# Optimization experiments

Measured on AMD Instinct MI355X. Metric: run time of the kernel, lower is better.

## Reference

```python
import jax, jax.numpy as jnp
import numpy as np

EMBED = 256
HEADS = 8
LEVELS = 3
POINTS = 4
MLP = 4
SS = np.array([[100, 100], [50, 50], [25, 25]], np.int32)  # (H, W) per level


def setup_inputs() -> dict:
    key = jax.random.key(0)
    ks = jax.random.split(key, 12)
    B, Q = 2, 128 * 128
    NV = int((SS[:, 0] * SS[:, 1]).sum())
    C = EMBED
    F = C * MLP
    s = 0.02

    def w(k, shape):
        return jax.random.normal(k, shape, jnp.float32) * s

    return dict(
        query=jax.random.normal(ks[0], (B, Q, C), jnp.float32),
        value=jax.random.normal(ks[1], (B, NV, C), jnp.float32),
        query_pos=jax.random.normal(ks[2], (B, Q, C), jnp.float32),
        ref_pts=jax.random.uniform(ks[3], (B, Q, 2), jnp.float32),
        spatial_shapes=SS,
        level_start_index=np.concatenate([[0], np.cumsum(SS[:, 0] * SS[:, 1])[:-1]]).astype(np.int32),
        ln1_g=jnp.ones(C), ln1_b=jnp.zeros(C),
        ln2_g=jnp.ones(C), ln2_b=jnp.zeros(C),
        W_value=w(ks[4], (C, C)), b_value=jnp.zeros(C),
        W_off=w(ks[5], (C, HEADS * LEVELS * POINTS * 2)), b_off=w(ks[6], (HEADS * LEVELS * POINTS * 2,)),
        W_attn=w(ks[7], (C, HEADS * LEVELS * POINTS)), b_attn=jnp.zeros(HEADS * LEVELS * POINTS),
        W_out=w(ks[8], (C, C)), b_out=jnp.zeros(C),
        W_ffn1=w(ks[9], (C, F)), b_ffn1=jnp.zeros(F),
        W_ffn2=w(ks[10], (F, C)), b_ffn2=jnp.zeros(C),
    )


def _layernorm(x, g, b, eps=1e-5):
    m = x.mean(-1, keepdims=True)
    v = ((x - m) ** 2).mean(-1, keepdims=True)
    return (x - m) * jax.lax.rsqrt(v + eps) * g + b


def _bilinear(v, loc, Hl, Wl):
    # v: [BH, Hl*Wl, d]; loc: [BH, Q, P, 2] normalized to [0,1].
    # grid_sample(align_corners=False, padding=zeros): pixel = loc*size - 0.5
    BH, Q, P, _ = loc.shape
    d = v.shape[-1]
    x = loc[..., 0] * Wl - 0.5
    y = loc[..., 1] * Hl - 0.5
    x0f = jnp.floor(x)
    y0f = jnp.floor(y)
    lx = x - x0f
    ly = y - y0f
    x0 = x0f.astype(jnp.int32)
    y0 = y0f.astype(jnp.int32)

    def gather(xi, yi):
        valid = ((xi >= 0) & (xi < Wl) & (yi >= 0) & (yi < Hl)).astype(v.dtype)
        idx = jnp.clip(yi, 0, Hl - 1) * Wl + jnp.clip(xi, 0, Wl - 1)
        g = jnp.take_along_axis(v, idx.reshape(BH, Q * P, 1), axis=1).reshape(BH, Q, P, d)
        return g * valid[..., None]

    w00 = (1 - lx) * (1 - ly)
    w01 = lx * (1 - ly)
    w10 = (1 - lx) * ly
    w11 = lx * ly
    return (gather(x0, y0) * w00[..., None] + gather(x0 + 1, y0) * w01[..., None]
            + gather(x0, y0 + 1) * w10[..., None] + gather(x0 + 1, y0 + 1) * w11[..., None])


def _forward(query, value, query_pos, ref_pts, spatial_shapes,
             ln1_g, ln1_b, ln2_g, ln2_b,
             W_value, b_value, W_off, b_off, W_attn, b_attn, W_out, b_out,
             W_ffn1, b_ffn1, W_ffn2, b_ffn2):
    B, Q, C = query.shape
    Hh, L, P = HEADS, LEVELS, POINTS
    d = C // Hh
    ss = np.asarray(spatial_shapes)
    starts = np.concatenate([[0], np.cumsum(ss[:, 0] * ss[:, 1])])

    # pre-norm + positional embedding (MSDeformAttn adds query_pos)
    qn = _layernorm(query, ln1_g, ln1_b)
    q = qn + query_pos

    # value projection, split heads
    v = (value @ W_value + b_value).reshape(B, -1, Hh, d)

    off = (q @ W_off + b_off).reshape(B, Q, Hh, L, P, 2)
    aw = jax.nn.softmax((q @ W_attn + b_attn).reshape(B, Q, Hh, L * P), axis=-1)
    aw = aw.reshape(B, Q, Hh, L, P)

    # offset normalizer is (W, H) per level
    normalizer = jnp.asarray(ss[:, ::-1].copy(), jnp.float32)
    # bev_value path: ref_pts broadcast over levels
    loc = ref_pts[:, :, None, None, None, :] + off / normalizer[None, None, None, :, None, :]

    out = jnp.zeros((B * Hh, Q, d), query.dtype)
    for l in range(L):
        Hl, Wl = int(ss[l, 0]), int(ss[l, 1])
        v_l = v[:, starts[l]:starts[l + 1]].transpose(0, 2, 1, 3).reshape(B * Hh, Hl * Wl, d)
        loc_l = loc[:, :, :, l].transpose(0, 2, 1, 3, 4).reshape(B * Hh, Q, P, 2)
        sampled = _bilinear(v_l, loc_l, Hl, Wl)  # [BH, Q, P, d]
        w_l = aw[:, :, :, l].transpose(0, 2, 1, 3).reshape(B * Hh, Q, P)
        out = out + (sampled * w_l[..., None]).sum(2)

    out = out.reshape(B, Hh, Q, d).transpose(0, 2, 1, 3).reshape(B, Q, C)
    x = query + (out @ W_out + b_out)

    h = _layernorm(x, ln2_g, ln2_b)
    x = x + (jax.nn.gelu(h @ W_ffn1 + b_ffn1, approximate=False) @ W_ffn2 + b_ffn2)
    return x


def reference(query, value, query_pos, ref_pts, spatial_shapes, level_start_index,
              ln1_g, ln1_b, ln2_g, ln2_b,
              W_value, b_value, W_off, b_off, W_attn, b_attn, W_out, b_out,
              W_ffn1, b_ffn1, W_ffn2, b_ffn2):
    return _forward(query, value, query_pos, ref_pts, spatial_shapes,
                    ln1_g, ln1_b, ln2_g, ln2_b,
                    W_value, b_value, W_off, b_off, W_attn, b_attn, W_out, b_out,
                    W_ffn1, b_ffn1, W_ffn2, b_ffn2)
```

## Files before the change

kernel.cpp:

```cpp
#include <hip/hip_runtime.h>
#include <hip/hip_bf16.h>

#define BQ      2
#define QLEN    16384
#define CDIM    256
#define HEADS   8
#define LEV     3
#define PTS     4
#define DHEAD   32
#define NVTOT   13125
#define FDIM    1024
#define NTOK    (BQ*QLEN)
#define MROWS_V (BQ*NVTOT)
#define NPROJ   288

typedef __attribute__((ext_vector_type(8))) short short8;
typedef __attribute__((ext_vector_type(4))) float floatx4;
typedef unsigned long long u64;

typedef const __attribute__((address_space(1))) unsigned int gu32;
typedef __attribute__((address_space(3))) unsigned int lu32;

__device__ __forceinline__ int imin(int a, int b){ return a<b?a:b; }
__device__ __forceinline__ int imax(int a, int b){ return a>b?a:b; }

__device__ __forceinline__ float bf2f(unsigned short u){ return __uint_as_float((unsigned)u << 16); }
__device__ __forceinline__ unsigned short f2bf(float f)
{
    __hip_bfloat16 h = __float2bfloat16(f);
    return *(unsigned short*)&h;
}
__device__ __forceinline__ u64 pack4(float4 v)
{
    return (u64)f2bf(v.x) | ((u64)f2bf(v.y) << 16)
         | ((u64)f2bf(v.z) << 32) | ((u64)f2bf(v.w) << 48);
}
__device__ __forceinline__ float4 unpack4(u64 c)
{
    float4 v;
    v.x = bf2f((unsigned short)(c));
    v.y = bf2f((unsigned short)(c >> 16));
    v.z = bf2f((unsigned short)(c >> 32));
    v.w = bf2f((unsigned short)(c >> 48));
    return v;
}

__device__ __forceinline__ float gelu_f(float x)
{
    float u2 = x * x;
    float a  = x * fmaf(0.0713548163f, u2, 1.5957691216f);
    float e  = __expf(a);
    float r  = __builtin_amdgcn_rcpf(e + 1.0f);
    return fmaf(-x, r, x);
}

__device__ __forceinline__ void ln_core(float4 v, const float* __restrict__ pos, int tok,
                                        const float* __restrict__ g, const float* __restrict__ b,
                                        int lane, __hip_bfloat16* __restrict__ out)
{
    float s = v.x + v.y + v.z + v.w;
    #pragma unroll
    for (int o = 32; o > 0; o >>= 1) s += __shfl_down(s, o);
    s = __shfl(s, 0);
    float mean = s * (1.0f / 256.0f);
    float4 c; c.x = v.x - mean; c.y = v.y - mean; c.z = v.z - mean; c.w = v.w - mean;
    float q2 = c.x*c.x + c.y*c.y + c.z*c.z + c.w*c.w;
    #pragma unroll
    for (int o = 32; o > 0; o >>= 1) q2 += __shfl_down(q2, o);
    q2 = __shfl(q2, 0);
    float rstd = rsqrtf(q2 * (1.0f / 256.0f) + 1e-5f);
    float4 gg = ((const float4*)g)[lane];
    float4 bb = ((const float4*)b)[lane];
    float4 o4;
    o4.x = c.x * rstd * gg.x + bb.x;
    o4.y = c.y * rstd * gg.y + bb.y;
    o4.z = c.z * rstd * gg.z + bb.z;
    o4.w = c.w * rstd * gg.w + bb.w;
    if (pos) {
        float4 p = ((const float4*)(pos + (size_t)tok * CDIM))[lane];
        o4.x += p.x; o4.y += p.y; o4.z += p.z; o4.w += p.w;
    }
    *(u64*)(out + (size_t)tok * CDIM + lane * 4) = pack4(o4);
}

#define WT_BLOCKS  2946
#define CVT_BLOCKS 6563
#define LN_BLOCKS  8192

__global__ __launch_bounds__(256)
void prep_k(const float* __restrict__ Wv,  const float* __restrict__ Woff,
            const float* __restrict__ Wat, const float* __restrict__ Wout,
            const float* __restrict__ W1,  const float* __restrict__ W2,
            const float* __restrict__ boff, const float* __restrict__ bat,
            const float* __restrict__ value, const float* __restrict__ query,
            const float* __restrict__ qpos,  const float* __restrict__ ln1g,
            const float* __restrict__ ln1b,
            __hip_bfloat16* __restrict__ o_v,  __hip_bfloat16* __restrict__ o_c,
            __hip_bfloat16* __restrict__ o_out,
            __hip_bfloat16* __restrict__ o_1,  __hip_bfloat16* __restrict__ o_2,
            float* __restrict__ o_bc,
            __hip_bfloat16* __restrict__ vbf,  __hip_bfloat16* __restrict__ qbf)
{
    int bx = blockIdx.x;
    if (bx < WT_BLOCKS) {
        int gid = bx * 256 + threadIdx.x;
        if (gid < 65536) {
            int idx = gid, n = idx >> 8, k = idx & 255;
            o_v[idx] = __float2bfloat16(Wv[(size_t)k * 256 + n]);
        } else if (gid < 163840) {
            int idx = gid - 65536, n = idx >> 8, k = idx & 255;
            float v = 0.0f;
            if (n < 192)       v = Woff[(size_t)k * 192 + n];
            else if (n < 288)  v = Wat[(size_t)k * 96 + (n - 192)];
            o_c[idx] = __float2bfloat16(v);
        } else if (gid < 229376) {
            int idx = gid - 163840, n = idx >> 8, k = idx & 255;
            o_out[idx] = __float2bfloat16(Wout[(size_t)k * 256 + n]);
        } else if (gid < 491520) {
            int idx = gid - 229376, n = idx >> 8, k = idx & 255;
            o_1[idx] = __float2bfloat16(W1[(size_t)k * 1024 + n]);
        } else if (gid < 753664) {
            int idx = gid - 491520, n = idx >> 10, k = idx & 1023;
            o_2[idx] = __float2bfloat16(W2[(size_t)k * 256 + n]);
        } else if (gid < 753952) {
            int idx = gid - 753664;
            o_bc[idx] = (idx < 192) ? boff[idx] : bat[idx - 192];
        }
    } else if (bx < WT_BLOCKS + CVT_BLOCKS) {
        int i = (bx - WT_BLOCKS) * 256 + threadIdx.x;
        if (i < MROWS_V * CDIM / 4) {
            float4 v = ((const float4*)value)[i];
            *(u64*)(vbf + (size_t)i * 4) = pack4(v);
        }
    } else {
        int tok  = (bx - WT_BLOCKS - CVT_BLOCKS) * 4 + (threadIdx.x >> 6);
        int lane = threadIdx.x & 63;
        float4 v = ((const float4*)(query + (size_t)tok * CDIM))[lane];
        ln_core(v, qpos, tok, ln1g, ln1b, lane, qbf);
    }
}

__global__ __launch_bounds__(256)
void ln2_k(const __hip_bfloat16* __restrict__ x, const float* __restrict__ g,
           const float* __restrict__ b, __hip_bfloat16* __restrict__ out)
{
    int tok  = blockIdx.x * 4 + (threadIdx.x >> 6);
    int lane = threadIdx.x & 63;
    float4 v = unpack4(((const u64*)(x + (size_t)tok * CDIM))[lane]);
    ln_core(v, nullptr, tok, g, b, lane, out);
}

enum { EP_PLAIN_BF16 = 0, EP_GELU_BF16 = 1, EP_RES_F2BF = 2, EP_RES_BF2F = 3 };

__global__ __launch_bounds__(256)
void mm_k(const __hip_bfloat16* __restrict__ A, const __hip_bfloat16* __restrict__ Bt,
          const float* __restrict__ bias, const void* __restrict__ res,
          void* __restrict__ Cout, int M, int N, int K, int mode)
{
    __shared__ float4 smem4[2048];
    __hip_bfloat16* Ws = (__hip_bfloat16*)smem4;
    __hip_bfloat16* Ts = (__hip_bfloat16*)smem4 + 128*64;
    u64* st = (u64*)smem4;
    int t = threadIdx.x;
    int lane = t & 63;
    int wave = t >> 6;
    int wm = wave >> 1, wn = wave & 1;
    int lm = lane & 15, lk = lane >> 4;
    int m0 = blockIdx.x * 128;
    int n0 = blockIdx.y * 128;

    floatx4 acc[4][4];
    #pragma unroll
    for (int i = 0; i < 4; i++)
        #pragma unroll
        for (int j = 0; j < 4; j++) acc[i][j] = (floatx4)0.0f;

    for (int kt = 0; kt < K; kt += 64) {
        #pragma unroll
        for (int i = 0; i < 4; i++) {
            int cc  = i * 256 + t;
            int row = cc >> 3;
            int c   = cc & 7;
            int kc  = c ^ (row & 7);
            int ra  = m0 + row; if (ra >= M) ra = M - 1;
            const __hip_bfloat16* gw = Bt + (size_t)(n0 + row) * K + kt + kc * 8;
            const __hip_bfloat16* gt = A  + (size_t)ra * K + kt + kc * 8;
            __builtin_amdgcn_global_load_lds((gu32*)gw, (lu32*)(Ws + cc * 8), 16, 0, 0);
            __builtin_amdgcn_global_load_lds((gu32*)gt, (lu32*)(Ts + cc * 8), 16, 0, 0);
        }
        __syncthreads();
        #pragma unroll
        for (int ks = 0; ks < 2; ks++) {
            short8 wf[4], tf[4];
            #pragma unroll
            for (int i = 0; i < 4; i++) {
                int rw = wn * 64 + i * 16 + lm;
                int cw = (ks * 4 + lk) ^ (rw & 7);
                wf[i] = *(const short8*)(Ws + (rw * 8 + cw) * 8);
                int rt = wm * 64 + i * 16 + lm;
                int ct = (ks * 4 + lk) ^ (rt & 7);
                tf[i] = *(const short8*)(Ts + (rt * 8 + ct) * 8);
            }
            #pragma unroll
            for (int i = 0; i < 4; i++)
                #pragma unroll
                for (int j = 0; j < 4; j++)
                    acc[i][j] = __builtin_amdgcn_mfma_f32_16x16x32_bf16(wf[i], tf[j], acc[i][j], 0, 0, 0);
        }
        __syncthreads();
    }

    #pragma unroll
    for (int i = 0; i < 4; i++) {
        int chan = n0 + wn * 64 + i * 16 + lk * 4;
        float4 b4 = make_float4(0.f, 0.f, 0.f, 0.f);
        if (chan < N) b4 = *(const float4*)(bias + chan);
        int c4 = wn * 16 + i * 4 + lk;
        #pragma unroll
        for (int j = 0; j < 4; j++) {
            int tl = wm * 64 + j * 16 + lm;
            float4 v;
            v.x = acc[i][j][0] + b4.x;
            v.y = acc[i][j][1] + b4.y;
            v.z = acc[i][j][2] + b4.z;
            v.w = acc[i][j][3] + b4.w;
            st[tl * 32 + (c4 ^ (tl & 31))] = pack4(v);
        }
    }
    __syncthreads();

    int rel = (t & 31) * 4;
    int c4r = t & 31;
    #pragma unroll
    for (int it = 0; it < 16; it++) {
        int tl   = it * 8 + (t >> 5);
        int tok  = m0 + tl;
        int chan = n0 + rel;
        if (tok >= M || chan >= N) continue;
        u64 chunk = st[tl * 32 + (c4r ^ (tl & 31))];
        if (mode == EP_PLAIN_BF16) {
            *(u64*)((__hip_bfloat16*)Cout + (size_t)tok * N + chan) = chunk;
        } else if (mode == EP_GELU_BF16) {
            float4 v = unpack4(chunk);
            v.x = gelu_f(v.x); v.y = gelu_f(v.y); v.z = gelu_f(v.z); v.w = gelu_f(v.w);
            *(u64*)((__hip_bfloat16*)Cout + (size_t)tok * N + chan) = pack4(v);
        } else if (mode == EP_RES_F2BF) {
            float4 v = unpack4(chunk);
            float4 rr = *(const float4*)((const float*)res + (size_t)tok * N + chan);
            v.x += rr.x; v.y += rr.y; v.z += rr.z; v.w += rr.w;
            *(u64*)((__hip_bfloat16*)Cout + (size_t)tok * N + chan) = pack4(v);
        } else {
            float4 v = unpack4(chunk);
            float4 rr = unpack4(*(const u64*)((const __hip_bfloat16*)res + (size_t)tok * N + chan));
            v.x += rr.x; v.y += rr.y; v.z += rr.z; v.w += rr.w;
            *(float4*)((float*)Cout + (size_t)tok * N + chan) = v;
        }
    }
}

__global__ __launch_bounds__(256, 6)
void sample_k(const __hip_bfloat16* __restrict__ v, const __hip_bfloat16* __restrict__ cbuf,
              const float* __restrict__ ref, __hip_bfloat16* __restrict__ out)
{
    __shared__ int4   metaIdx[4 * 104];
    __shared__ float4 metaW[4 * 104];

    int wid  = threadIdx.x >> 6;
    int lane = threadIdx.x & 63;
    int t    = blockIdx.x * 4 + wid;
    int b    = t >> 14;
    float rx = ref[(size_t)t * 2 + 0];
    float ry = ref[(size_t)t * 2 + 1];
    const __hip_bfloat16* crow = cbuf + (size_t)t * NPROJ;

    #pragma unroll
    for (int rnd = 0; rnd < 2; rnd++) {
        int slot = rnd * 64 + lane;
        int h = slot >> 4, p = slot & 15;
        int pc = imin(p, 11);
        unsigned upk = *(const unsigned*)(crow + h * 24 + pc * 2);
        float ox = bf2f((unsigned short)upk);
        float oy = bf2f((unsigned short)(upk >> 16));
        float logit = bf2f(*(const unsigned short*)(crow + 192 + h * 12 + pc));
        float mx = logit;
        #pragma unroll
        for (int o = 8; o > 0; o >>= 1) mx = fmaxf(mx, __shfl_xor(mx, o, 16));
        float e = (p < 12) ? __expf(logit - mx) : 0.0f;
        float ssum = e;
        #pragma unroll
        for (int o = 8; o > 0; o >>= 1) ssum += __shfl_xor(ssum, o, 16);
        float aw = e * __builtin_amdgcn_rcpf(ssum);

        if (p < 12) {
            int l = p >> 2;
            float fS = (l == 0) ? 100.0f : ((l == 1) ? 50.0f : 25.0f);
            int   Wl = (l == 0) ? 100 : ((l == 1) ? 50 : 25);
            int   st = (l == 0) ? 0 : ((l == 1) ? 10000 : 12500);
            float x = fmaf(rx, fS, ox) - 0.5f;
            float y = fmaf(ry, fS, oy) - 0.5f;
            float x0f = floorf(x), y0f = floorf(y);
            float fx = x - x0f, fy = y - y0f;
            int x0 = (int)x0f, y0 = (int)y0f;
            int x1 = x0 + 1,  y1 = y0 + 1;
            int cx0 = imin(imax(x0, 0), Wl - 1), cx1 = imin(imax(x1, 0), Wl - 1);
            int cy0 = imin(imax(y0, 0), Wl - 1), cy1 = imin(imax(y1, 0), Wl - 1);
            float vx0 = (x0 >= 0 && x0 < Wl) ? 1.0f : 0.0f;
            float vx1 = (x1 >= 0 && x1 < Wl) ? 1.0f : 0.0f;
            float vy0 = (y0 >= 0 && y0 < Wl) ? 1.0f : 0.0f;
            float vy1 = (y1 >= 0 && y1 < Wl) ? 1.0f : 0.0f;
            int s = wid * 104 + h * 13 + p;
            metaIdx[s] = make_int4((st + cy0 * Wl + cx0) << 9, (st + cy0 * Wl + cx1) << 9,
                                   (st + cy1 * Wl + cx0) << 9, (st + cy1 * Wl + cx1) << 9);
            metaW[s] = make_float4((1.0f - fx) * (1.0f - fy) * aw * vx0 * vy0,
                                   fx * (1.0f - fy) * aw * vx1 * vy0,
                                   (1.0f - fx) * fy * aw * vx0 * vy1,
                                   fx * fy * aw * vx1 * vy1);
        }
    }
    __syncthreads();

    int h  = lane >> 3;
    int bs = __builtin_amdgcn_readfirstlane(b);
    const char* vb = (const char*)(v + (size_t)bs * NVTOT * CDIM);
    int hoff = lane * 8;
    int sB   = wid * 104 + h * 13;
    float4 acc = {0.0f, 0.0f, 0.0f, 0.0f};

    int4   miA = metaIdx[sB + 0];
    float4 mwA = metaW[sB + 0];
    u64 a0 = *(const u64*)(vb + (unsigned)(miA.x + hoff));
    u64 a1 = *(const u64*)(vb + (unsigned)(miA.y + hoff));
    u64 a2 = *(const u64*)(vb + (unsigned)(miA.z + hoff));
    u64 a3 = *(const u64*)(vb + (unsigned)(miA.w + hoff));
    int4   miB = metaIdx[sB + 1];
    float4 mwB = metaW[sB + 1];
    u64 b0 = *(const u64*)(vb + (unsigned)(miB.x + hoff));
    u64 b1 = *(const u64*)(vb + (unsigned)(miB.y + hoff));
    u64 b2 = *(const u64*)(vb + (unsigned)(miB.z + hoff));
    u64 b3 = *(const u64*)(vb + (unsigned)(miB.w + hoff));

    #pragma unroll
    for (int p = 0; p < 12; p++) {
        int pn = (p < 10) ? (p + 2) : 11;
        int4   miN = metaIdx[sB + pn];
        float4 mwN = metaW[sB + pn];
        u64 n0 = *(const u64*)(vb + (unsigned)(miN.x + hoff));
        u64 n1 = *(const u64*)(vb + (unsigned)(miN.y + hoff));
        u64 n2 = *(const u64*)(vb + (unsigned)(miN.z + hoff));
        u64 n3 = *(const u64*)(vb + (unsigned)(miN.w + hoff));

        {
            unsigned d0 = (unsigned)a0, d1 = (unsigned)(a0 >> 32);
            acc.x = fmaf(mwA.x, __uint_as_float(d0 << 16), acc.x);
            acc.y = fmaf(mwA.x, __uint_as_float(d0 & 0xffff0000u), acc.y);
            acc.z = fmaf(mwA.x, __uint_as_float(d1 << 16), acc.z);
            acc.w = fmaf(mwA.x, __uint_as_float(d1 & 0xffff0000u), acc.w);
        }
        {
            unsigned d0 = (unsigned)a1, d1 = (unsigned)(a1 >> 32);
            acc.x = fmaf(mwA.y, __uint_as_float(d0 << 16), acc.x);
            acc.y = fmaf(mwA.y, __uint_as_float(d0 & 0xffff0000u), acc.y);
            acc.z = fmaf(mwA.y, __uint_as_float(d1 << 16), acc.z);
            acc.w = fmaf(mwA.y, __uint_as_float(d1 & 0xffff0000u), acc.w);
        }
        {
            unsigned d0 = (unsigned)a2, d1 = (unsigned)(a2 >> 32);
            acc.x = fmaf(mwA.z, __uint_as_float(d0 << 16), acc.x);
            acc.y = fmaf(mwA.z, __uint_as_float(d0 & 0xffff0000u), acc.y);
            acc.z = fmaf(mwA.z, __uint_as_float(d1 << 16), acc.z);
            acc.w = fmaf(mwA.z, __uint_as_float(d1 & 0xffff0000u), acc.w);
        }
        {
            unsigned d0 = (unsigned)a3, d1 = (unsigned)(a3 >> 32);
            acc.x = fmaf(mwA.w, __uint_as_float(d0 << 16), acc.x);
            acc.y = fmaf(mwA.w, __uint_as_float(d0 & 0xffff0000u), acc.y);
            acc.z = fmaf(mwA.w, __uint_as_float(d1 << 16), acc.z);
            acc.w = fmaf(mwA.w, __uint_as_float(d1 & 0xffff0000u), acc.w);
        }

        a0 = b0; a1 = b1; a2 = b2; a3 = b3; mwA = mwB;
        b0 = n0; b1 = n1; b2 = n2; b3 = n3; mwB = mwN;
    }
    *(u64*)(out + (size_t)t * CDIM + lane * 4) = pack4(acc);
}

extern "C" void kernel_launch(void* const* d_in, const int* in_sizes, int n_in,
                              void* d_out, int out_size, void* d_ws, size_t ws_size,
                              hipStream_t stream)
{
    const float* query = (const float*)d_in[0];
    const float* value = (const float*)d_in[1];
    const float* qpos  = (const float*)d_in[2];
    const float* ref   = (const float*)d_in[3];
    const float* ln1g  = (const float*)d_in[6];
    const float* ln1b  = (const float*)d_in[7];
    const float* ln2g  = (const float*)d_in[8];
    const float* ln2b  = (const float*)d_in[9];
    const float* Wv    = (const float*)d_in[10];
    const float* bv    = (const float*)d_in[11];
    const float* Woff  = (const float*)d_in[12];
    const float* boff  = (const float*)d_in[13];
    const float* Wat   = (const float*)d_in[14];
    const float* bat   = (const float*)d_in[15];
    const float* Wout  = (const float*)d_in[16];
    const float* bout  = (const float*)d_in[17];
    const float* W1    = (const float*)d_in[18];
    const float* b1    = (const float*)d_in[19];
    const float* W2    = (const float*)d_in[20];
    const float* b2    = (const float*)d_in[21];
    float* out = (float*)d_out;
    char*  ws  = (char*)d_ws;

    const size_t MB = 1024 * 1024;
    __hip_bfloat16* Wvt   = (__hip_bfloat16*)(ws + 0);
    __hip_bfloat16* Wct   = (__hip_bfloat16*)(ws + 131072);
    __hip_bfloat16* Woutt = (__hip_bfloat16*)(ws + 327680);
    __hip_bfloat16* W1t   = (__hip_bfloat16*)(ws + 458752);
    __hip_bfloat16* W2t   = (__hip_bfloat16*)(ws + 983040);
    float*          bcomb = (float*)(ws + 1507328);
    __hip_bfloat16* qbf   = (__hip_bfloat16*)(ws + 2  * MB);
    __hip_bfloat16* aoutb = (__hip_bfloat16*)(ws + 19 * MB);
    __hip_bfloat16* vbf   = (__hip_bfloat16*)(ws + 36 * MB);
    __hip_bfloat16* vbuf  = (__hip_bfloat16*)(ws + 50 * MB);
    __hip_bfloat16* xbf   = (__hip_bfloat16*)(ws + 64 * MB);
    __hip_bfloat16* cbuf  = (__hip_bfloat16*)(ws + 81 * MB);
    __hip_bfloat16* gbf   = (__hip_bfloat16*)(ws + 100 * MB);
    __hip_bfloat16* hbf   = qbf;

    prep_k<<<WT_BLOCKS + CVT_BLOCKS + LN_BLOCKS, 256, 0, stream>>>(
        Wv, Woff, Wat, Wout, W1, W2, boff, bat, value, query, qpos, ln1g, ln1b,
        Wvt, Wct, Woutt, W1t, W2t, bcomb, vbf, qbf);
    mm_k<<<dim3((MROWS_V + 127) / 128, 2), 256, 0, stream>>>(
        vbf, Wvt, bv, nullptr, vbuf, MROWS_V, 256, 256, EP_PLAIN_BF16);
    mm_k<<<dim3(NTOK / 128, 3), 256, 0, stream>>>(
        qbf, Wct, bcomb, nullptr, cbuf, NTOK, NPROJ, 256, EP_PLAIN_BF16);
    sample_k<<<NTOK / 4, 256, 0, stream>>>(vbuf, cbuf, ref, aoutb);
    mm_k<<<dim3(NTOK / 128, 2), 256, 0, stream>>>(
        aoutb, Woutt, bout, query, xbf, NTOK, 256, 256, EP_RES_F2BF);
    ln2_k<<<NTOK / 4, 256, 0, stream>>>(xbf, ln2g, ln2b, hbf);
    mm_k<<<dim3(NTOK / 128, 8), 256, 0, stream>>>(
        hbf, W1t, b1, nullptr, gbf, NTOK, FDIM, 256, EP_GELU_BF16);
    mm_k<<<dim3(NTOK / 128, 2), 256, 0, stream>>>(
        gbf, W2t, b2, xbf, out, NTOK, 256, 1024, EP_RES_BF2F);
}
```

Measured before the change: 355.1 us.

## Fuse FFN up-projection, GELU and down-projection into one kernel

Replaces the two FFN GEMM launches with a single kernel. Each 128-token block keeps its LN2 output tile in LDS, computes 128-wide chunks of the hidden layer with GELU into a double-buffered LDS tile, and accumulates the down-projection in registers, adding bias and residual at the end. This removes the round trip of the 1024-wide bf16 hidden activation through global memory. In exchange it needs 128KB of dynamic LDS per block, which limits occupancy, and only 256 blocks are launched. Weight fragments are loaded straight from global memory in every chunk without LDS staging.

```diff
diff --git a/kernel.cpp b/kernel.cpp
--- a/kernel.cpp
+++ b/kernel.cpp
@@ -258,6 +258,152 @@
     }
 }
 
+__global__ __launch_bounds__(512, 2)
+void ffn_k(const __hip_bfloat16* __restrict__ h,
+           const __hip_bfloat16* __restrict__ W1t,
+           const float* __restrict__ b1,
+           const __hip_bfloat16* __restrict__ W2t,
+           const float* __restrict__ b2,
+           const __hip_bfloat16* __restrict__ xres,
+           float* __restrict__ out)
+{
+    extern __shared__ char smem_dyn[];
+    __hip_bfloat16* As = (__hip_bfloat16*)smem_dyn;
+
+    int t    = threadIdx.x;
+    int lane = t & 63;
+    int wave = t >> 6;
+    int wm   = wave >> 2;
+    int wn   = wave & 3;
+    int lm   = lane & 15, lk = lane >> 4;
+    int m0   = blockIdx.x * 128;
+
+    #pragma unroll
+    for (int i = 0; i < 8; i++) {
+        int cc  = i * 512 + t;
+        int kt  = cc >> 10;
+        int rem = cc & 1023;
+        int row = rem >> 3;
+        int c   = rem & 7;
+        int kc  = c ^ (row & 7);
+        const __hip_bfloat16* src = h + (size_t)(m0 + row) * 256 + kt * 64 + kc * 8;
+        __builtin_amdgcn_global_load_lds((gu32*)src, (lu32*)(As + cc * 8), 16, 0, 0);
+    }
+
+    floatx4 acc2[4][4];
+    #pragma unroll
+    for (int i = 0; i < 4; i++)
+        #pragma unroll
+        for (int j = 0; j < 4; j++) acc2[i][j] = (floatx4)0.0f;
+
+    __syncthreads();
+
+    #pragma unroll 1
+    for (int fc = 0; fc < 8; fc++) {
+        int f0 = fc * 128;
+        __hip_bfloat16* gs = (__hip_bfloat16*)(smem_dyn + 65536 + (fc & 1) * 32768);
+
+        floatx4 acc1[2][4];
+        #pragma unroll
+        for (int i = 0; i < 2; i++)
+            #pragma unroll
+            for (int j = 0; j < 4; j++) acc1[i][j] = (floatx4)0.0f;
+
+        short8 w1f[8][2];
+        #pragma unroll
+        for (int kt = 0; kt < 4; kt++)
+            #pragma unroll
+            for (int ks = 0; ks < 2; ks++)
+                #pragma unroll
+                for (int i = 0; i < 2; i++)
+                    w1f[kt * 2 + ks][i] = *(const short8*)(W1t
+                        + (size_t)(f0 + wn * 32 + i * 16 + lm) * 256
+                        + kt * 64 + ks * 32 + lk * 8);
+
+        #pragma unroll
+        for (int kt = 0; kt < 4; kt++) {
+            #pragma unroll
+            for (int ks = 0; ks < 2; ks++) {
+                short8 tf[4];
+                #pragma unroll
+                for (int j = 0; j < 4; j++) {
+                    int rt = wm * 64 + j * 16 + lm;
+                    int ct = (ks * 4 + lk) ^ (rt & 7);
+                    tf[j] = *(const short8*)(As + (kt * 1024 + rt * 8 + ct) * 8);
+                }
+                #pragma unroll
+                for (int i = 0; i < 2; i++)
+                    #pragma unroll
+                    for (int j = 0; j < 4; j++)
+                        acc1[i][j] = __builtin_amdgcn_mfma_f32_16x16x32_bf16(
+                            w1f[kt * 2 + ks][i], tf[j], acc1[i][j], 0, 0, 0);
+            }
+        }
+
+        #pragma unroll
+        for (int i = 0; i < 2; i++) {
+            float4 bb = *(const float4*)(b1 + f0 + wn * 32 + i * 16 + lk * 4);
+            int c = wn * 4 + i * 2 + (lk >> 1);
+            #pragma unroll
+            for (int j = 0; j < 4; j++) {
+                int tok = wm * 64 + j * 16 + lm;
+                float4 v;
+                v.x = gelu_f(acc1[i][j][0] + bb.x);
+                v.y = gelu_f(acc1[i][j][1] + bb.y);
+                v.z = gelu_f(acc1[i][j][2] + bb.z);
+                v.w = gelu_f(acc1[i][j][3] + bb.w);
+                int sc = c ^ (tok & 7);
+                *(u64*)((char*)gs + tok * 256 + sc * 16 + (lk & 1) * 8) = pack4(v);
+            }
+        }
+
+        short8 w2f[4][4];
+        #pragma unroll
+        for (int ks2 = 0; ks2 < 4; ks2++)
+            #pragma unroll
+            for (int i2 = 0; i2 < 4; i2++)
+                w2f[ks2][i2] = *(const short8*)(W2t
+                    + (size_t)(wn * 64 + i2 * 16 + lm) * 1024
+                    + f0 + ks2 * 32 + lk * 8);
+
+        __syncthreads();
+
+        #pragma unroll
+        for (int ks2 = 0; ks2 < 4; ks2++) {
+            short8 tf2[4];
+            #pragma unroll
+            for (int j = 0; j < 4; j++) {
+                int tok = wm * 64 + j * 16 + lm;
+                int sc = (ks2 * 4 + lk) ^ (tok & 7);
+                tf2[j] = *(const short8*)((char*)gs + tok * 256 + sc * 16);
+            }
+            #pragma unroll
+            for (int i2 = 0; i2 < 4; i2++)
+                #pragma unroll
+                for (int j = 0; j < 4; j++)
+                    acc2[i2][j] = __builtin_amdgcn_mfma_f32_16x16x32_bf16(
+                        w2f[ks2][i2], tf2[j], acc2[i2][j], 0, 0, 0);
+        }
+    }
+
+    #pragma unroll
+    for (int i2 = 0; i2 < 4; i2++) {
+        int c0 = wn * 64 + i2 * 16 + lk * 4;
+        float4 bb = *(const float4*)(b2 + c0);
+        #pragma unroll
+        for (int j = 0; j < 4; j++) {
+            int tok = m0 + wm * 64 + j * 16 + lm;
+            float4 r = unpack4(*(const u64*)(xres + (size_t)tok * 256 + c0));
+            float4 v;
+            v.x = acc2[i2][j][0] + bb.x + r.x;
+            v.y = acc2[i2][j][1] + bb.y + r.y;
+            v.z = acc2[i2][j][2] + bb.z + r.z;
+            v.w = acc2[i2][j][3] + bb.w + r.w;
+            *(float4*)(out + (size_t)tok * 256 + c0) = v;
+        }
+    }
+}
+
 __global__ __launch_bounds__(256, 6)
 void sample_k(const __hip_bfloat16* __restrict__ v, const __hip_bfloat16* __restrict__ cbuf,
               const float* __restrict__ ref, __hip_bfloat16* __restrict__ out)
@@ -411,6 +557,13 @@
     float* out = (float*)d_out;
     char*  ws  = (char*)d_ws;
 
+    static bool attr_set = false;
+    if (!attr_set) {
+        hipFuncSetAttribute((const void*)ffn_k,
+                            hipFuncAttributeMaxDynamicSharedMemorySize, 131072);
+        attr_set = true;
+    }
+
     const size_t MB = 1024 * 1024;
     __hip_bfloat16* Wvt   = (__hip_bfloat16*)(ws + 0);
     __hip_bfloat16* Wct   = (__hip_bfloat16*)(ws + 131072);
@@ -424,7 +577,6 @@
     __hip_bfloat16* vbuf  = (__hip_bfloat16*)(ws + 50 * MB);
     __hip_bfloat16* xbf   = (__hip_bfloat16*)(ws + 64 * MB);
     __hip_bfloat16* cbuf  = (__hip_bfloat16*)(ws + 81 * MB);
-    __hip_bfloat16* gbf   = (__hip_bfloat16*)(ws + 100 * MB);
     __hip_bfloat16* hbf   = qbf;
 
     prep_k<<<WT_BLOCKS + CVT_BLOCKS + LN_BLOCKS, 256, 0, stream>>>(
@@ -438,8 +590,5 @@
     mm_k<<<dim3(NTOK / 128, 2), 256, 0, stream>>>(
         aoutb, Woutt, bout, query, xbf, NTOK, 256, 256, EP_RES_F2BF);
     ln2_k<<<NTOK / 4, 256, 0, stream>>>(xbf, ln2g, ln2b, hbf);
-    mm_k<<<dim3(NTOK / 128, 8), 256, 0, stream>>>(
-        hbf, W1t, b1, nullptr, gbf, NTOK, FDIM, 256, EP_GELU_BF16);
-    mm_k<<<dim3(NTOK / 128, 2), 256, 0, stream>>>(
-        gbf, W2t, b2, xbf, out, NTOK, 256, 1024, EP_RES_BF2F);
-}
+    ffn_k<<<NTOK / 128, 512, 131072, stream>>>(hbf, W1t, b1, W2t, b2, xbf, out);
+}
```

After: 352.8 us. Within noise of the previous version (-0.7%).
